# Optimization experiments

Hardware: AMD Instinct MI355X
Metric: run time of the kernel (lower is better)

Reference implementation:

```python
import jax, jax.numpy as jnp
import numpy as np

D_MODEL = 1024
N_HEADS = 16
D_HEAD = 64
TOTAL = N_HEADS * D_HEAD


def setup_inputs() -> dict:
    key = jax.random.key(0)
    k1, k2, k3 = jax.random.split(key, 3)
    x = jax.random.normal(k1, (2, 2048, D_MODEL), dtype=jnp.float32)
    W_qkv = jax.random.normal(k2, (3 * TOTAL, D_MODEL), dtype=jnp.float32) * 0.02
    W_out = jax.random.normal(k3, (D_MODEL, TOTAL), dtype=jnp.float32) * 0.02
    return {"x": x, "W_qkv": W_qkv, "W_out": W_out}


def reference(x, W_qkv, W_out):
    B, T, D = x.shape
    scale = D_HEAD ** -0.5
    qkv = jnp.einsum('btd,ed->bte', x, W_qkv)  # [B,T,3*TOTAL]
    q, k, v = jnp.split(qkv, 3, axis=-1)
    def heads(t):
        return t.reshape(B, T, N_HEADS, D_HEAD).transpose(0, 2, 1, 3)  # [B,H,T,Dh]
    q, k, v = heads(q), heads(k), heads(v)
    scores = jnp.einsum('bhqd,bhkd->bhqk', q, k) * scale
    causal = jnp.tril(jnp.ones((T, T), dtype=bool))
    scores = jnp.where(causal[None, None], scores, -jnp.inf)
    attn = jax.nn.softmax(scores, axis=-1)
    out = jnp.einsum('bhqk,bhkd->bhqd', attn, v)
    out = out.transpose(0, 2, 1, 3).reshape(B, T, TOTAL)
    return jnp.einsum('bte,de->btd', out, W_out)
```

## Files before the change

kernel.cpp:

```cpp
#include <hip/hip_runtime.h>
#include <hip/hip_bf16.h>

typedef __attribute__((ext_vector_type(4))) float f32x4;
typedef __attribute__((ext_vector_type(8))) short s16x8;
typedef __attribute__((ext_vector_type(4))) short s16x4;

#define DEV static __device__ __forceinline__

DEV unsigned short f2bf(float f) {
    unsigned int u = __builtin_bit_cast(unsigned int, f);
    u += 0x7fffu + ((u >> 16) & 1u);
    return (unsigned short)(u >> 16);
}

#if __has_builtin(__builtin_amdgcn_exp2f)
#define EXP2(x) __builtin_amdgcn_exp2f(x)
#else
#define EXP2(x) exp2f(x)
#endif

DEV unsigned int pack2(float a, float b) {
#if __has_builtin(__builtin_amdgcn_perm)
    return __builtin_amdgcn_perm(__builtin_bit_cast(unsigned int, b),
                                 __builtin_bit_cast(unsigned int, a), 0x07060302u);
#else
    return (__builtin_bit_cast(unsigned int, a) >> 16) |
           (__builtin_bit_cast(unsigned int, b) & 0xffff0000u);
#endif
}

DEV s16x8 ld8(const unsigned short* p) {
    s16x4 lo = *(const s16x4*)(p);
    s16x4 hi = *(const s16x4*)(p + 4);
    return __builtin_shufflevector(lo, hi, 0, 1, 2, 3, 4, 5, 6, 7);
}
DEV s16x8 ld8a(const unsigned short* p) { return *(const s16x8*)p; }

DEV f32x4 mfma16(s16x8 a, s16x8 b, f32x4 c) {
    return __builtin_amdgcn_mfma_f32_16x16x32_bf16(a, b, c, 0, 0, 0);
}

DEV void glds16(const unsigned short* g, unsigned short* l) {
    __builtin_amdgcn_global_load_lds(
        (const __attribute__((address_space(1))) unsigned int*)g,
        (__attribute__((address_space(3))) unsigned int*)l, 16, 0, 0);
}

__global__ __launch_bounds__(256) void convf2b2(
        const float* __restrict__ s0, unsigned short* __restrict__ d0, int n40,
        const float* __restrict__ s1, unsigned short* __restrict__ d1, int n41) {
    int i = blockIdx.x * 256 + threadIdx.x;
    if (i < n40) {
        float4 v = ((const float4*)s0)[i];
        s16x4 o = {(short)f2bf(v.x), (short)f2bf(v.y), (short)f2bf(v.z), (short)f2bf(v.w)};
        ((s16x4*)d0)[i] = o;
    } else if (i - n40 < n41) {
        int j = i - n40;
        float4 v = ((const float4*)s1)[j];
        s16x4 o = {(short)f2bf(v.x), (short)f2bf(v.y), (short)f2bf(v.z), (short)f2bf(v.w)};
        ((s16x4*)d1)[j] = o;
    }
}

__global__ __launch_bounds__(256) void convf2b(const float* __restrict__ s,
                                               unsigned short* __restrict__ d, int n4) {
    int i = blockIdx.x * 256 + threadIdx.x;
    if (i < n4) {
        float4 v = ((const float4*)s)[i];
        s16x4 o = {(short)f2bf(v.x), (short)f2bf(v.y), (short)f2bf(v.z), (short)f2bf(v.w)};
        ((s16x4*)d)[i] = o;
    }
}

__global__ __launch_bounds__(512) void qkv_gemm(
        const unsigned short* __restrict__ Xb, const unsigned short* __restrict__ Wq,
        unsigned short* __restrict__ q_ws, unsigned short* __restrict__ k_ws,
        unsigned short* __restrict__ v_ws) {
    __shared__ unsigned short As[2][128 * 32];
    __shared__ unsigned short Bs[2][128 * 32];
    const int tid = threadIdx.x, lane = tid & 63, wave = tid >> 6;
    const int l15 = lane & 15, l4 = lane >> 4;
    const int wm = (wave >> 1) * 32, wn = (wave & 1) * 64;
    const int m0 = blockIdx.y * 128, n0 = blockIdx.x * 128;

    f32x4 acc[2][4];
    for (int i = 0; i < 2; i++)
        for (int j = 0; j < 4; j++) acc[i][j] = (f32x4){0.f, 0.f, 0.f, 0.f};

    const unsigned short* aptr = &Xb[(size_t)(m0 + wave * 16 + (lane >> 2)) * 1024 + (lane & 3) * 8];
    const unsigned short* bptr = &Wq[(size_t)(n0 + wave * 16 + (lane >> 2)) * 1024 + (lane & 3) * 8];

    for (int k0 = 0; k0 < 1024; k0 += 64) {
        __syncthreads();
        for (int c = 0; c < 2; c++) {
            glds16(aptr + k0 + c * 32, &As[c][(wave * 16) * 32]);
            glds16(bptr + k0 + c * 32, &Bs[c][(wave * 16) * 32]);
        }
        __syncthreads();
        for (int c = 0; c < 2; c++) {
            s16x8 af[2], bf[4];
            for (int mt = 0; mt < 2; mt++) af[mt] = ld8a(&As[c][(wm + mt * 16 + l15) * 32 + l4 * 8]);
            for (int nt = 0; nt < 4; nt++) bf[nt] = ld8a(&Bs[c][(wn + nt * 16 + l15) * 32 + l4 * 8]);
            for (int mt = 0; mt < 2; mt++)
                for (int nt = 0; nt < 4; nt++)
                    acc[mt][nt] = mfma16(af[mt], bf[nt], acc[mt][nt]);
        }
    }

    const int gnb = n0 + wn;
    const int which = gnb >> 10, h = (gnb >> 6) & 15;
    const int bidx = m0 >> 11, tb = m0 & 2047;
    if (which == 2) {
        unsigned short* dst = v_ws + (size_t)(bidx * 16 + h) * 64 * 2048;
        for (int mt = 0; mt < 2; mt++) {
            int t = tb + wm + mt * 16 + l4 * 4;
            for (int nt = 0; nt < 4; nt++) {
                int dh = nt * 16 + l15;
                s16x4 pp;
                for (int r = 0; r < 4; r++) pp[r] = (short)f2bf(acc[mt][nt][r]);
                *(s16x4*)&dst[(size_t)dh * 2048 + t] = pp;
            }
        }
    } else {
        unsigned short* dst = ((which == 0) ? q_ws : k_ws) + (size_t)(bidx * 16 + h) * 2048 * 64;
        const float sc = (which == 0) ? 0.18033688f : 1.0f;
        for (int mt = 0; mt < 2; mt++) {
            int t0 = tb + wm + mt * 16 + l4 * 4;
            for (int nt = 0; nt < 4; nt++) {
                int dh = nt * 16 + l15;
                for (int r = 0; r < 4; r++)
                    dst[(size_t)(t0 + r) * 64 + dh] = f2bf(acc[mt][nt][r] * sc);
            }
        }
    }
}

__global__ __launch_bounds__(512) void attn(
        const unsigned short* __restrict__ q_ws, const unsigned short* __restrict__ k_ws,
        const unsigned short* __restrict__ v_ws, unsigned short* __restrict__ ao) {
    constexpr int LDP = 68;
    __shared__ unsigned short Ks[2][2][64 * 32];
    __shared__ unsigned short Vt[2][2][64 * 32];
    __shared__ unsigned short Ps[8 * 16 * LDP];
    const int tid = threadIdx.x, lane = tid & 63, wave = tid >> 6;
    const int l15 = lane & 15, l4 = lane >> 4;
    const int bh = blockIdx.x, b = bh >> 4, h = bh & 15;
    const int q0 = (15 - blockIdx.y) * 128;
    const int qw0 = q0 + wave * 16;
    const size_t base = (size_t)bh * 2048 * 64;
    const unsigned short* vtb = v_ws + (size_t)bh * 64 * 2048;
    unsigned short* Pw = &Ps[wave * 16 * LDP];

    const int seg = wave & 3, half = wave >> 2;
    const unsigned short* kg0 = &k_ws[base + (size_t)(seg * 16 + (lane >> 2)) * 64 + half * 32 + (lane & 3) * 8];
    const unsigned short* vg0 = &vtb[(size_t)(seg * 16 + (lane >> 2)) * 2048 + half * 32 + (lane & 3) * 8];
    unsigned short* kl[2] = {&Ks[0][half][(seg * 16) * 32], &Ks[1][half][(seg * 16) * 32]};
    unsigned short* vl[2] = {&Vt[0][half][(seg * 16) * 32], &Vt[1][half][(seg * 16) * 32]};

    s16x8 qf[2];
    for (int c = 0; c < 2; c++)
        qf[c] = ld8a(&q_ws[base + (size_t)(qw0 + l15) * 64 + c * 32 + l4 * 8]);

    f32x4 o[4];
    for (int i = 0; i < 4; i++) o[i] = (f32x4){0.f, 0.f, 0.f, 0.f};
    float lsum = 0.f;

    glds16(kg0, kl[0]);
    glds16(vg0, vl[0]);

    const int kend = q0 + 128;
    for (int k0 = 0; k0 < kend; k0 += 64) {
        const int cur = (k0 >> 6) & 1;
        __syncthreads();
        if (k0 + 64 < kend) {
            glds16(kg0 + (size_t)(k0 + 64) * 64, kl[cur ^ 1]);
            glds16(vg0 + (k0 + 64), vl[cur ^ 1]);
        }

        if (k0 < qw0 + 16) {
            f32x4 st[4];
            for (int ks = 0; ks < 4; ks++) st[ks] = (f32x4){0.f, 0.f, 0.f, 0.f};
            for (int c = 0; c < 2; c++)
                for (int ks = 0; ks < 4; ks++) {
                    s16x8 kf = ld8a(&Ks[cur][c][(ks * 16 + l15) * 32 + l4 * 8]);
                    st[ks] = mfma16(kf, qf[c], st[ks]);
                }

            if (k0 + 63 > qw0) {
                int qg = qw0 + l15;
                for (int ks = 0; ks < 4; ks++)
                    for (int r = 0; r < 4; r++) {
                        int kg = k0 + ks * 16 + l4 * 4 + r;
                        if (kg > qg) st[ks][r] = -1e30f;
                    }
            }
            float part = 0.f;
            for (int ks = 0; ks < 4; ks++) {
                float p0 = EXP2(st[ks][0]);
                float p1 = EXP2(st[ks][1]);
                float p2 = EXP2(st[ks][2]);
                float p3 = EXP2(st[ks][3]);
                part += (p0 + p1) + (p2 + p3);
                unsigned int u0 = pack2(p0, p1), u1 = pack2(p2, p3);
                *(uint2*)&Pw[l15 * LDP + ks * 16 + l4 * 4] = (uint2){u0, u1};
            }
            lsum += part;

            s16x8 pf[2];
            for (int c = 0; c < 2; c++)
                pf[c] = ld8(&Pw[l15 * LDP + c * 32 + l4 * 8]);
            for (int c = 0; c < 2; c++)
                for (int ds = 0; ds < 4; ds++) {
                    s16x8 vf = ld8a(&Vt[cur][c][(ds * 16 + l15) * 32 + l4 * 8]);
                    o[ds] = mfma16(vf, pf[c], o[ds]);
                }
        }
    }

    float t = lsum;
    t += __shfl_xor(t, 16, 64);
    t += __shfl_xor(t, 32, 64);
    float inv = 1.f / t;
    for (int ds = 0; ds < 4; ds++) {
        s16x4 pp;
        for (int r = 0; r < 4; r++) pp[r] = (short)f2bf(o[ds][r] * inv);
        *(s16x4*)&Pw[l15 * LDP + ds * 16 + l4 * 4] = pp;
    }
    int qr = lane >> 2, qt = lane & 3;
    size_t orow = ((size_t)b * 2048 + q0 + wave * 16 + qr) * 1024 + h * 64 + qt * 16;
    *(s16x8*)&ao[orow]     = ld8(&Pw[qr * LDP + qt * 16]);
    *(s16x8*)&ao[orow + 8] = ld8(&Pw[qr * LDP + qt * 16 + 8]);
}

__global__ __launch_bounds__(256) void out_gemm(
        const unsigned short* __restrict__ A, const unsigned short* __restrict__ Bm,
        float* __restrict__ OUT) {
    __shared__ unsigned short As[2][128 * 32];
    __shared__ unsigned short Bs[2][64 * 32];
    const int tid = threadIdx.x, lane = tid & 63, wave = tid >> 6;
    const int l15 = lane & 15, l4 = lane >> 4;
    const int wm = wave * 32;
    const int m0 = blockIdx.y * 128, n0 = blockIdx.x * 64;

    f32x4 acc[2][4];
    for (int i = 0; i < 2; i++)
        for (int j = 0; j < 4; j++) acc[i][j] = (f32x4){0.f, 0.f, 0.f, 0.f};

    const unsigned short* aptr = &A[(size_t)(m0 + wave * 32 + (lane >> 2)) * 1024 + (lane & 3) * 8];
    const unsigned short* bptr = &Bm[(size_t)(n0 + wave * 16 + (lane >> 2)) * 1024 + (lane & 3) * 8];

    for (int k0 = 0; k0 < 1024; k0 += 64) {
        __syncthreads();
        for (int c = 0; c < 2; c++) {
            glds16(aptr + k0 + c * 32, &As[c][(wave * 32) * 32]);
            glds16(aptr + k0 + c * 32 + 16 * 1024, &As[c][(wave * 32 + 16) * 32]);
            glds16(bptr + k0 + c * 32, &Bs[c][(wave * 16) * 32]);
        }
        __syncthreads();
        for (int c = 0; c < 2; c++) {
            s16x8 af[2], bf[4];
            for (int mt = 0; mt < 2; mt++) af[mt] = ld8a(&As[c][(wm + mt * 16 + l15) * 32 + l4 * 8]);
            for (int nt = 0; nt < 4; nt++) bf[nt] = ld8a(&Bs[c][(nt * 16 + l15) * 32 + l4 * 8]);
            for (int mt = 0; mt < 2; mt++)
                for (int nt = 0; nt < 4; nt++)
                    acc[mt][nt] = mfma16(af[mt], bf[nt], acc[mt][nt]);
        }
    }

    for (int mt = 0; mt < 2; mt++)
        for (int nt = 0; nt < 4; nt++)
            for (int r = 0; r < 4; r++) {
                int gm = m0 + wm + mt * 16 + l4 * 4 + r;
                int gn = n0 + nt * 16 + l15;
                OUT[(size_t)gm * 1024 + gn] = acc[mt][nt][r];
            }
}

extern "C" void kernel_launch(void* const* d_in, const int* in_sizes, int n_in,
                              void* d_out, int out_size, void* d_ws, size_t ws_size,
                              hipStream_t stream) {
    (void)in_sizes; (void)n_in; (void)out_size; (void)ws_size;
    const float* x    = (const float*)d_in[0];
    const float* Wqkv = (const float*)d_in[1];
    const float* Wout = (const float*)d_in[2];
    float* out = (float*)d_out;

    unsigned short* q_ws = (unsigned short*)d_ws;
    unsigned short* k_ws = q_ws + (size_t)4 * 1024 * 1024;
    unsigned short* v_ws = k_ws + (size_t)4 * 1024 * 1024;
    unsigned short* xb   = v_ws + (size_t)4 * 1024 * 1024;
    unsigned short* ao   = xb;
    unsigned short* wqb  = (unsigned short*)d_out;
    unsigned short* wob  = q_ws;

    const int n4x = 2 * 2048 * 1024 / 4, n4w = 3072 * 1024 / 4;
    convf2b2<<<(n4x + n4w + 255) / 256, 256, 0, stream>>>(x, xb, n4x, Wqkv, wqb, n4w);
    qkv_gemm<<<dim3(24, 32), 512, 0, stream>>>(xb, wqb, q_ws, k_ws, v_ws);
    attn<<<dim3(32, 16), 512, 0, stream>>>(q_ws, k_ws, v_ws, ao);
    convf2b<<<1024, 256, 0, stream>>>(Wout, wob, 1024 * 1024 / 4);
    out_gemm<<<dim3(16, 32), 256, 0, stream>>>(ao, wob, out);
}
```

Before: 170.0 us.

## Fuse W_out bf16 conversion into out_gemm and remap GEMM tiles per XCD

Removes the separate convf2b launch for W_out. out_gemm now loads fp32 weights directly, converts them to bf16 in registers and writes them to a padded LDS tile, replacing the async global-to-LDS copy for B. Both GEMMs also remap block indices so that blocks assigned to the same XCD share nearby M/N tiles, which should improve L2 reuse. The trade-off is that out_gemm reads twice the weight bytes, and each of the 32 M-tile blocks converts the same weights again; the B-tile loads are also now synchronous register loads rather than async LDS loads.

Result: no change. 170.4 us (+0.2%).

```diff
diff --git a/kernel.cpp b/kernel.cpp
--- a/kernel.cpp
+++ b/kernel.cpp
@@ -62,16 +62,6 @@
     }
 }
 
-__global__ __launch_bounds__(256) void convf2b(const float* __restrict__ s,
-                                               unsigned short* __restrict__ d, int n4) {
-    int i = blockIdx.x * 256 + threadIdx.x;
-    if (i < n4) {
-        float4 v = ((const float4*)s)[i];
-        s16x4 o = {(short)f2bf(v.x), (short)f2bf(v.y), (short)f2bf(v.z), (short)f2bf(v.w)};
-        ((s16x4*)d)[i] = o;
-    }
-}
-
 __global__ __launch_bounds__(512) void qkv_gemm(
         const unsigned short* __restrict__ Xb, const unsigned short* __restrict__ Wq,
         unsigned short* __restrict__ q_ws, unsigned short* __restrict__ k_ws,
@@ -81,7 +71,10 @@
     const int tid = threadIdx.x, lane = tid & 63, wave = tid >> 6;
     const int l15 = lane & 15, l4 = lane >> 4;
     const int wm = (wave >> 1) * 32, wn = (wave & 1) * 64;
-    const int m0 = blockIdx.y * 128, n0 = blockIdx.x * 128;
+    const int linear = blockIdx.y * 24 + blockIdx.x;
+    const int xcd = linear & 7, s = linear >> 3;
+    const int m0 = ((xcd >> 1) * 8 + (s & 7)) * 128;
+    const int n0 = ((xcd & 1) * 12 + (s >> 3)) * 128;
 
     f32x4 acc[2][4];
     for (int i = 0; i < 2; i++)
@@ -233,34 +226,55 @@
 }
 
 __global__ __launch_bounds__(256) void out_gemm(
-        const unsigned short* __restrict__ A, const unsigned short* __restrict__ Bm,
+        const unsigned short* __restrict__ A, const float* __restrict__ W,
         float* __restrict__ OUT) {
+    constexpr int LDB = 36;
     __shared__ unsigned short As[2][128 * 32];
-    __shared__ unsigned short Bs[2][64 * 32];
+    __shared__ unsigned short Bs[2][64 * LDB];
     const int tid = threadIdx.x, lane = tid & 63, wave = tid >> 6;
     const int l15 = lane & 15, l4 = lane >> 4;
     const int wm = wave * 32;
-    const int m0 = blockIdx.y * 128, n0 = blockIdx.x * 64;
+    const int linear = blockIdx.y * 16 + blockIdx.x;
+    const int xcd = linear & 7, s = linear >> 3;
+    const int m0 = ((xcd >> 1) * 8 + (s & 7)) * 128;
+    const int n0 = ((xcd & 1) * 8 + (s >> 3)) * 64;
 
     f32x4 acc[2][4];
     for (int i = 0; i < 2; i++)
         for (int j = 0; j < 4; j++) acc[i][j] = (f32x4){0.f, 0.f, 0.f, 0.f};
 
     const unsigned short* aptr = &A[(size_t)(m0 + wave * 32 + (lane >> 2)) * 1024 + (lane & 3) * 8];
-    const unsigned short* bptr = &Bm[(size_t)(n0 + wave * 16 + (lane >> 2)) * 1024 + (lane & 3) * 8];
+    const int brow = wave * 16 + (lane >> 2), bsub = lane & 3;
+    const float* bptr = &W[(size_t)(n0 + brow) * 1024 + bsub * 16];
+    const int bc = bsub >> 1;
+    const int bcol = (bsub & 1) * 16;
+    unsigned short* bdst = &Bs[bc][brow * LDB + bcol];
 
     for (int k0 = 0; k0 < 1024; k0 += 64) {
+        float4 w0 = *(const float4*)(bptr + k0);
+        float4 w1 = *(const float4*)(bptr + k0 + 4);
+        float4 w2 = *(const float4*)(bptr + k0 + 8);
+        float4 w3 = *(const float4*)(bptr + k0 + 12);
         __syncthreads();
         for (int c = 0; c < 2; c++) {
             glds16(aptr + k0 + c * 32, &As[c][(wave * 32) * 32]);
             glds16(aptr + k0 + c * 32 + 16 * 1024, &As[c][(wave * 32 + 16) * 32]);
-            glds16(bptr + k0 + c * 32, &Bs[c][(wave * 16) * 32]);
+        }
+        {
+            uint2 lo = {pack2(w0.x, w0.y), pack2(w0.z, w0.w)};
+            uint2 hi = {pack2(w1.x, w1.y), pack2(w1.z, w1.w)};
+            *(uint2*)(bdst)     = lo;
+            *(uint2*)(bdst + 4) = hi;
+            uint2 lo2 = {pack2(w2.x, w2.y), pack2(w2.z, w2.w)};
+            uint2 hi2 = {pack2(w3.x, w3.y), pack2(w3.z, w3.w)};
+            *(uint2*)(bdst + 8)  = lo2;
+            *(uint2*)(bdst + 12) = hi2;
         }
         __syncthreads();
         for (int c = 0; c < 2; c++) {
             s16x8 af[2], bf[4];
             for (int mt = 0; mt < 2; mt++) af[mt] = ld8a(&As[c][(wm + mt * 16 + l15) * 32 + l4 * 8]);
-            for (int nt = 0; nt < 4; nt++) bf[nt] = ld8a(&Bs[c][(nt * 16 + l15) * 32 + l4 * 8]);
+            for (int nt = 0; nt < 4; nt++) bf[nt] = ld8(&Bs[c][(nt * 16 + l15) * LDB + l4 * 8]);
             for (int mt = 0; mt < 2; mt++)
                 for (int nt = 0; nt < 4; nt++)
                     acc[mt][nt] = mfma16(af[mt], bf[nt], acc[mt][nt]);
@@ -291,12 +305,10 @@
     unsigned short* xb   = v_ws + (size_t)4 * 1024 * 1024;
     unsigned short* ao   = xb;
     unsigned short* wqb  = (unsigned short*)d_out;
-    unsigned short* wob  = q_ws;
 
     const int n4x = 2 * 2048 * 1024 / 4, n4w = 3072 * 1024 / 4;
     convf2b2<<<(n4x + n4w + 255) / 256, 256, 0, stream>>>(x, xb, n4x, Wqkv, wqb, n4w);
     qkv_gemm<<<dim3(24, 32), 512, 0, stream>>>(xb, wqb, q_ws, k_ws, v_ws);
     attn<<<dim3(32, 16), 512, 0, stream>>>(q_ws, k_ws, v_ws, ao);
-    convf2b<<<1024, 256, 0, stream>>>(Wout, wob, 1024 * 1024 / 4);
-    out_gemm<<<dim3(16, 32), 256, 0, stream>>>(ao, wob, out);
-}
+    out_gemm<<<dim3(16, 32), 256, 0, stream>>>(ao, Wout, out);
+}
```
